# Kernel optimization log

Hardware: AMD Instinct MI355X
Metric: run time of the kernel (lower is better)

Reference implementation:

```python
import jax, jax.numpy as jnp
import numpy as np

STATE_DIM = 4
HIDDEN = 64
N_SAMPLES = 32768
N_STEPS = 512
DT = 0.01


def _xavier(key, shape):
    fan_in, fan_out = shape
    lim = float(np.sqrt(6.0 / (fan_in + fan_out)))
    return jax.random.uniform(key, shape, jnp.float32, -lim, lim)


def _lipswish(x):
    return 0.909 * x * jax.nn.sigmoid(x)


def _mlp(y, W1, b1, W2, b2, W3, b3, W4, b4):
    h = _lipswish(y @ W1 + b1)
    h = _lipswish(h @ W2 + b2)
    h = _lipswish(h @ W3 + b3)
    return h @ W4 + b4


def setup_inputs() -> dict:
    key = jax.random.key(0)
    ks = jax.random.split(key, 10)
    inp = {
        "initial_states": jax.random.normal(ks[0], (N_SAMPLES, STATE_DIM), jnp.float32),
        "times": jnp.arange(N_STEPS, dtype=jnp.float32) * DT,
        "noise": jax.random.normal(ks[1], (N_STEPS - 1, N_SAMPLES, STATE_DIM), jnp.float32),
    }
    # f_net and g_net parameters (xavier_uniform weights, zero biases)
    for prefix, base in (("f", 2), ("g", 6)):
        kk = jax.random.split(ks[base], 4)
        shapes = [(STATE_DIM, HIDDEN), (HIDDEN, HIDDEN), (HIDDEN, HIDDEN), (HIDDEN, STATE_DIM)]
        for i, s in enumerate(shapes):
            inp[f"{prefix}W{i+1}"] = _xavier(kk[i], s)
            inp[f"{prefix}b{i+1}"] = jnp.zeros((s[1],), jnp.float32)
    return inp


def reference(initial_states, times, noise,
              fW1, fb1, fW2, fb2, fW3, fb3, fW4, fb4,
              gW1, gb1, gW2, gb2, gW3, gb3, gW4, gb4):
    dts = times[1:] - times[:-1]  # [T-1]

    def step(y, inp):
        dt, dw = inp
        drift = jnp.clip(_mlp(y, fW1, fb1, fW2, fb2, fW3, fb3, fW4, fb4), -100.0, 100.0)
        diff = jnp.maximum(jax.nn.softplus(_mlp(y, gW1, gb1, gW2, gb2, gW3, gb3, gW4, gb4)), 1e-4)
        y_next = y + drift * dt + diff * jnp.sqrt(dt) * dw  # Euler-Maruyama, diagonal noise
        return y_next, y_next

    _, ys = jax.lax.scan(step, initial_states, (dts, noise))  # [T-1, N, D]
    traj = jnp.concatenate([initial_states[None], ys], axis=0)  # [T, N, D]
    return jnp.transpose(traj, (1, 0, 2))  # [N, T, D]
```

## Files before the change

kernel.cpp:

```cpp
#include <hip/hip_runtime.h>
#include <hip/hip_bf16.h>

#define NS 32768
#define NT 512
#define HD 64

#define WS_NET 8900
#define WS_DTS 17800
#define WS_SQ 18311
#define WS_FLAG 18822

struct P16 { const void* p[16]; };

__global__ void prep_kernel(P16 wp, const void* timesp, float* ws) {
  unsigned first = ((const unsigned*)timesp)[0];
  bool isbf = (first != 0u);
  int tid = blockIdx.x * blockDim.x + threadIdx.x;
  int stride = gridDim.x * blockDim.x;
  for (int idx = tid; idx < WS_DTS + (NT - 1); idx += stride) {
    if (idx < WS_DTS) {
      int net = (idx >= WS_NET) ? 1 : 0;
      int r = idx - net * WS_NET;
      int ti, src;
      if (r < 256) {
        int jg = r >> 6, rem = r & 63, k = rem >> 4, jj = rem & 15;
        ti = 0; src = k * 64 + jg * 16 + jj;
      } else if (r < 320) {
        ti = 1; src = r - 256;
      } else if (r < 4416) {
        int rr = r - 320; int jg = rr >> 10, rem = rr & 1023, k = rem >> 4, jj = rem & 15;
        ti = 2; src = k * 64 + jg * 16 + jj;
      } else if (r < 4480) {
        ti = 3; src = r - 4416;
      } else if (r < 8576) {
        int rr = r - 4480; int jg = rr >> 10, rem = rr & 1023, k = rem >> 4, jj = rem & 15;
        ti = 4; src = k * 64 + jg * 16 + jj;
      } else if (r < 8640) {
        ti = 5; src = r - 8576;
      } else if (r < 8896) {
        ti = 6; src = r - 8640;
      } else {
        ti = 7; src = r - 8896;
      }
      ti += net * 8;
      float v = isbf ? __bfloat162float(((const __hip_bfloat16*)wp.p[ti])[src])
                     : ((const float*)wp.p[ti])[src];
      ws[idx] = v;
    } else {
      int t = idx - WS_DTS;
      float t0, t1;
      if (isbf) {
        t0 = __bfloat162float(((const __hip_bfloat16*)timesp)[t]);
        t1 = __bfloat162float(((const __hip_bfloat16*)timesp)[t + 1]);
      } else {
        t0 = ((const float*)timesp)[t];
        t1 = ((const float*)timesp)[t + 1];
      }
      float dt = t1 - t0;
      ws[WS_DTS + t] = dt;
      ws[WS_SQ + t] = sqrtf(dt);
    }
  }
  if (blockIdx.x == 0 && threadIdx.x == 0) ws[WS_FLAG] = isbf ? 1.0f : 0.0f;
}

__device__ __forceinline__ float lipswish(float x) {
  float e = __expf(-x);
  return 0.909f * x * __builtin_amdgcn_rcpf(1.0f + e);
}

__device__ __forceinline__ unsigned short f2bs(float x) {
  return __bfloat16_as_ushort(__float2bfloat16(x));
}

__device__ __forceinline__ void store_out(void* outp, bool isbf, int sample, int t,
                                          const float v[4]) {
  if (isbf) {
    uint2 u;
    u.x = (unsigned)f2bs(v[0]) | ((unsigned)f2bs(v[1]) << 16);
    u.y = (unsigned)f2bs(v[2]) | ((unsigned)f2bs(v[3]) << 16);
    ((uint2*)outp)[(size_t)sample * NT + t] = u;
  } else {
    float4 f = make_float4(v[0], v[1], v[2], v[3]);
    ((float4*)outp)[(size_t)sample * NT + t] = f;
  }
}

__global__ __launch_bounds__(512, 4) void sde_kernel(
    const void* __restrict__ y0p, const void* __restrict__ noisep,
    const float* __restrict__ ws, void* __restrict__ outp) {
  const int tid = threadIdx.x;
  const int lane = tid & 63;
  const int uwv = __builtin_amdgcn_readfirstlane(tid >> 6);
  const int unet = uwv >> 2;
  const int ujg = uwv & 3;
  const int j0 = ujg * 16;
  const int sample = blockIdx.x * 64 + lane;
  const bool isbf = (ws[WS_FLAG] != 0.0f);

  const float* Wb = ws + unet * WS_NET;
  const float* W1p = Wb + ujg * 64;
  const float* b1p = Wb + 256 + ujg * 16;
  const float* W2p = Wb + 320 + ujg * 1024;
  const float* b2p = Wb + 4416 + ujg * 16;
  const float* W3p = Wb + 4480 + ujg * 1024;
  const float* b3p = Wb + 8576 + ujg * 16;
  const float* W4p = Wb + 8640 + ujg * 64;
  const float* b4 = Wb + 8896;
  const float* dts = ws + WS_DTS;
  const float* sqdts = ws + WS_SQ;

  __shared__ float h[2][2][HD][64];
  __shared__ float exch[2][8][4][64];

  float y[4];
  if (isbf) {
    const __hip_bfloat16* y0 = (const __hip_bfloat16*)y0p;
#pragma unroll
    for (int d = 0; d < 4; ++d) y[d] = __bfloat162float(y0[sample * 4 + d]);
  } else {
    const float* y0 = (const float*)y0p;
#pragma unroll
    for (int d = 0; d < 4; ++d) y[d] = y0[sample * 4 + d];
  }

  if (uwv == 0) store_out(outp, isbf, sample, 0, y);

  for (int t = 0; t < NT - 1; ++t) {
    float dw[4];
    if (isbf) {
      uint2 nz = ((const uint2*)noisep)[(size_t)t * NS + sample];
      dw[0] = __uint_as_float((nz.x & 0xffffu) << 16);
      dw[1] = __uint_as_float(nz.x & 0xffff0000u);
      dw[2] = __uint_as_float((nz.y & 0xffffu) << 16);
      dw[3] = __uint_as_float(nz.y & 0xffff0000u);
    } else {
      float4 nz = ((const float4*)noisep)[(size_t)t * NS + sample];
      dw[0] = nz.x; dw[1] = nz.y; dw[2] = nz.z; dw[3] = nz.w;
    }

    float a[16];
#pragma unroll
    for (int jj = 0; jj < 16; ++jj)
      a[jj] = b1p[jj] + y[0] * W1p[jj] + y[1] * W1p[16 + jj] + y[2] * W1p[32 + jj] +
              y[3] * W1p[48 + jj];
#pragma unroll
    for (int jj = 0; jj < 16; ++jj) h[0][unet][j0 + jj][lane] = lipswish(a[jj]);
    __syncthreads();

#pragma unroll
    for (int jj = 0; jj < 16; ++jj) a[jj] = b2p[jj];
#pragma unroll 4
    for (int k = 0; k < HD; ++k) {
      float hk = h[0][unet][k][lane];
      const float* wr = W2p + k * 16;
#pragma unroll
      for (int jj = 0; jj < 16; ++jj) a[jj] = fmaf(hk, wr[jj], a[jj]);
    }
#pragma unroll
    for (int jj = 0; jj < 16; ++jj) h[1][unet][j0 + jj][lane] = lipswish(a[jj]);
    __syncthreads();

#pragma unroll
    for (int jj = 0; jj < 16; ++jj) a[jj] = b3p[jj];
#pragma unroll 4
    for (int k = 0; k < HD; ++k) {
      float hk = h[1][unet][k][lane];
      const float* wr = W3p + k * 16;
#pragma unroll
      for (int jj = 0; jj < 16; ++jj) a[jj] = fmaf(hk, wr[jj], a[jj]);
    }

    float o[4];
#pragma unroll
    for (int d = 0; d < 4; ++d) o[d] = (ujg == 0) ? b4[d] : 0.0f;
#pragma unroll
    for (int kk = 0; kk < 16; ++kk) {
      float hk = lipswish(a[kk]);
      const float* wr = W4p + kk * 4;
#pragma unroll
      for (int d = 0; d < 4; ++d) o[d] = fmaf(hk, wr[d], o[d]);
    }

    const int slot = t & 1;
#pragma unroll
    for (int d = 0; d < 4; ++d) exch[slot][uwv][d][lane] = o[d];
    __syncthreads();

    const float dt = dts[t];
    const float sq = sqdts[t];
#pragma unroll
    for (int d = 0; d < 4; ++d) {
      float fsum = (exch[slot][0][d][lane] + exch[slot][1][d][lane]) +
                   (exch[slot][2][d][lane] + exch[slot][3][d][lane]);
      float gsum = (exch[slot][4][d][lane] + exch[slot][5][d][lane]) +
                   (exch[slot][6][d][lane] + exch[slot][7][d][lane]);
      float drift = fminf(fmaxf(fsum, -100.0f), 100.0f);
      float sp = fmaxf(gsum, 0.0f) + log1pf(__expf(-fabsf(gsum)));
      float diff = fmaxf(sp, 1e-4f);
      y[d] = y[d] + drift * dt + diff * sq * dw[d];
    }

    if (uwv == 0) store_out(outp, isbf, sample, t + 1, y);
  }
}

extern "C" void kernel_launch(void* const* d_in, const int* in_sizes, int n_in,
                              void* d_out, int out_size, void* d_ws, size_t ws_size,
                              hipStream_t stream) {
  P16 wp;
  for (int i = 0; i < 16; ++i) wp.p[i] = d_in[3 + i];
  float* ws = (float*)d_ws;
  hipLaunchKernelGGL(prep_kernel, dim3(80), dim3(256), 0, stream, wp, d_in[1], ws);
  hipLaunchKernelGGL(sde_kernel, dim3(NS / 64), dim3(512), 0, stream, d_in[0], d_in[2],
                     ws, d_out);
}
```

Baseline: 12.00 ms.

## Use packed v2f FMAs, single-buffer hidden LDS, and raise occupancy bound

```diff
diff --git a/kernel.cpp b/kernel.cpp
--- a/kernel.cpp
+++ b/kernel.cpp
@@ -9,6 +9,8 @@
 #define WS_DTS 17800
 #define WS_SQ 18311
 #define WS_FLAG 18822
+
+typedef float v2f __attribute__((ext_vector_type(2)));
 
 struct P16 { const void* p[16]; };
 
@@ -86,7 +88,7 @@
   }
 }
 
-__global__ __launch_bounds__(512, 4) void sde_kernel(
+__global__ __launch_bounds__(512, 6) void sde_kernel(
     const void* __restrict__ y0p, const void* __restrict__ noisep,
     const float* __restrict__ ws, void* __restrict__ outp) {
   const int tid = threadIdx.x;
@@ -110,7 +112,7 @@
   const float* dts = ws + WS_DTS;
   const float* sqdts = ws + WS_SQ;
 
-  __shared__ float h[2][2][HD][64];
+  __shared__ float h[2][HD][64];
   __shared__ float exch[2][8][4][64];
 
   float y[4];
@@ -139,52 +141,74 @@
       dw[0] = nz.x; dw[1] = nz.y; dw[2] = nz.z; dw[3] = nz.w;
     }
 
-    float a[16];
-#pragma unroll
-    for (int jj = 0; jj < 16; ++jj)
-      a[jj] = b1p[jj] + y[0] * W1p[jj] + y[1] * W1p[16 + jj] + y[2] * W1p[32 + jj] +
-              y[3] * W1p[48 + jj];
-#pragma unroll
-    for (int jj = 0; jj < 16; ++jj) h[0][unet][j0 + jj][lane] = lipswish(a[jj]);
-    __syncthreads();
-
-#pragma unroll
-    for (int jj = 0; jj < 16; ++jj) a[jj] = b2p[jj];
+    v2f a[8];
+#pragma unroll
+    for (int c = 0; c < 8; ++c) a[c] = *(const v2f*)(b1p + 2 * c);
+#pragma unroll
+    for (int k = 0; k < 4; ++k) {
+      v2f yk = {y[k], y[k]};
+      const v2f* wr = (const v2f*)(W1p + k * 16);
+#pragma unroll
+      for (int c = 0; c < 8; ++c) a[c] = __builtin_elementwise_fma(yk, wr[c], a[c]);
+    }
+#pragma unroll
+    for (int c = 0; c < 8; ++c) {
+      h[unet][j0 + 2 * c][lane] = lipswish(a[c][0]);
+      h[unet][j0 + 2 * c + 1][lane] = lipswish(a[c][1]);
+    }
+    __syncthreads();
+
+#pragma unroll
+    for (int c = 0; c < 8; ++c) a[c] = *(const v2f*)(b2p + 2 * c);
 #pragma unroll 4
     for (int k = 0; k < HD; ++k) {
-      float hk = h[0][unet][k][lane];
-      const float* wr = W2p + k * 16;
-#pragma unroll
-      for (int jj = 0; jj < 16; ++jj) a[jj] = fmaf(hk, wr[jj], a[jj]);
-    }
-#pragma unroll
-    for (int jj = 0; jj < 16; ++jj) h[1][unet][j0 + jj][lane] = lipswish(a[jj]);
-    __syncthreads();
-
-#pragma unroll
-    for (int jj = 0; jj < 16; ++jj) a[jj] = b3p[jj];
+      float hk = h[unet][k][lane];
+      v2f hk2 = {hk, hk};
+      const v2f* wr = (const v2f*)(W2p + k * 16);
+#pragma unroll
+      for (int c = 0; c < 8; ++c) a[c] = __builtin_elementwise_fma(hk2, wr[c], a[c]);
+    }
+    __syncthreads();
+#pragma unroll
+    for (int c = 0; c < 8; ++c) {
+      h[unet][j0 + 2 * c][lane] = lipswish(a[c][0]);
+      h[unet][j0 + 2 * c + 1][lane] = lipswish(a[c][1]);
+    }
+    __syncthreads();
+
+#pragma unroll
+    for (int c = 0; c < 8; ++c) a[c] = *(const v2f*)(b3p + 2 * c);
 #pragma unroll 4
     for (int k = 0; k < HD; ++k) {
-      float hk = h[1][unet][k][lane];
-      const float* wr = W3p + k * 16;
-#pragma unroll
-      for (int jj = 0; jj < 16; ++jj) a[jj] = fmaf(hk, wr[jj], a[jj]);
-    }
-
-    float o[4];
-#pragma unroll
-    for (int d = 0; d < 4; ++d) o[d] = (ujg == 0) ? b4[d] : 0.0f;
+      float hk = h[unet][k][lane];
+      v2f hk2 = {hk, hk};
+      const v2f* wr = (const v2f*)(W3p + k * 16);
+#pragma unroll
+      for (int c = 0; c < 8; ++c) a[c] = __builtin_elementwise_fma(hk2, wr[c], a[c]);
+    }
+
+    v2f oA, oB;
+    if (ujg == 0) {
+      oA = *(const v2f*)(b4 + 0);
+      oB = *(const v2f*)(b4 + 2);
+    } else {
+      oA = (v2f){0.f, 0.f};
+      oB = (v2f){0.f, 0.f};
+    }
 #pragma unroll
     for (int kk = 0; kk < 16; ++kk) {
-      float hk = lipswish(a[kk]);
-      const float* wr = W4p + kk * 4;
-#pragma unroll
-      for (int d = 0; d < 4; ++d) o[d] = fmaf(hk, wr[d], o[d]);
+      float h3 = lipswish(a[kk >> 1][kk & 1]);
+      v2f h2 = {h3, h3};
+      const v2f* wr = (const v2f*)(W4p + kk * 4);
+      oA = __builtin_elementwise_fma(h2, wr[0], oA);
+      oB = __builtin_elementwise_fma(h2, wr[1], oB);
     }
 
     const int slot = t & 1;
-#pragma unroll
-    for (int d = 0; d < 4; ++d) exch[slot][uwv][d][lane] = o[d];
+    exch[slot][uwv][0][lane] = oA[0];
+    exch[slot][uwv][1][lane] = oA[1];
+    exch[slot][uwv][2][lane] = oB[0];
+    exch[slot][uwv][3][lane] = oB[1];
     __syncthreads();
 
     const float dt = dts[t];
```

Result: no change. 12.22 ms (+1.9%).
